# Optimization experiments

Measured on AMD Instinct MI355X. Metric: run time of the kernel, lower is better.

## Reference

```python
import jax, jax.numpy as jnp
import numpy as np

N_NODES = 50000
N_EDGES = 500000
D_MODEL = 256
N_HEADS = 8
D_K = D_MODEL // N_HEADS


def setup_inputs() -> dict:
    key = jax.random.key(0)
    ks = jax.random.split(key, 12)
    s = 1.0 / np.sqrt(D_MODEL)
    inp = {
        "query": jax.random.normal(ks[0], (N_NODES, D_MODEL), dtype=jnp.float32),
        "key": jax.random.normal(ks[1], (N_NODES, D_MODEL), dtype=jnp.float32),
        "value": jax.random.normal(ks[2], (N_NODES, D_MODEL), dtype=jnp.float32),
        "edges": jax.random.randint(ks[3], (2, N_EDGES), 0, N_NODES, dtype=jnp.int64),
        # four nn.Linear(d_model, d_model) layers: q, k, v, out
        "Wq": jax.random.uniform(ks[4], (D_MODEL, D_MODEL), jnp.float32, -s, s),
        "bq": jax.random.uniform(ks[5], (D_MODEL,), jnp.float32, -s, s),
        "Wk": jax.random.uniform(ks[6], (D_MODEL, D_MODEL), jnp.float32, -s, s),
        "bk": jax.random.uniform(ks[7], (D_MODEL,), jnp.float32, -s, s),
        "Wv": jax.random.uniform(ks[8], (D_MODEL, D_MODEL), jnp.float32, -s, s),
        "bv": jax.random.uniform(ks[9], (D_MODEL,), jnp.float32, -s, s),
        "Wo": jax.random.uniform(ks[10], (D_MODEL, D_MODEL), jnp.float32, -s, s),
        "bo": jax.random.uniform(ks[11], (D_MODEL,), jnp.float32, -s, s),
    }
    return inp


def reference(query, key, value, edges, Wq, bq, Wk, bk, Wv, bv, Wo, bo):
    N = query.shape[0]
    # linear projections (torch Linear: x @ W.T + b), view as [N, h, d_k]
    q = (query @ Wq.T + bq).reshape(N, N_HEADS, D_K)
    k = (key @ Wk.T + bk).reshape(N, N_HEADS, D_K)
    v = (value @ Wv.T + bv).reshape(N, N_HEADS, D_K)

    dst, src = edges[0], edges[1]
    # per-edge dot-product scores [E, h]
    scores = jnp.einsum("ehd,ehd->eh", q[dst], k[src]) / jnp.sqrt(
        jnp.asarray(D_K, dtype=q.dtype)
    )
    # segment softmax over destination node neighborhoods (per head)
    m = jax.ops.segment_max(scores, dst, num_segments=N)  # [N, h]
    ex = jnp.exp(scores - m[dst])
    den = jax.ops.segment_sum(ex, dst, num_segments=N)  # [N, h]
    p_attn = ex / den[dst]  # [E, h]

    # weighted scatter-sum of gathered values -> [N, h, d_k]
    out = jax.ops.segment_sum(p_attn[:, :, None] * v[src], dst, num_segments=N)
    out = out.reshape(N, D_MODEL)
    return out @ Wo.T + bo
```

## Files before the change

### kernel.cpp

```cpp
#include <hip/hip_runtime.h>
#include <hip/hip_bf16.h>
#include <cstdint>

#define D_MODEL 256
#define NHEADS 8
#define DK 32
#define LDSPAD 8
#define LDSROW (D_MODEL + LDSPAD)
#define LDSROWF (D_MODEL + 4)
#define PBLK 170

typedef float f32x4 __attribute__((ext_vector_type(4)));
typedef __bf16 bf16x8 __attribute__((ext_vector_type(8)));
typedef unsigned short u16x8 __attribute__((ext_vector_type(8)));

__device__ __forceinline__ unsigned short f2bf_rne(float f) {
    unsigned int u = __float_as_uint(f);
    u += 0x7FFF + ((u >> 16) & 1);
    return (unsigned short)(u >> 16);
}
__device__ __forceinline__ float bf2f(unsigned short h) {
    return __uint_as_float(((unsigned int)h) << 16);
}

__global__ void conv_weights_hist(const float* __restrict__ W0, const float* __restrict__ W1,
                                  const float* __restrict__ W2, const float* __restrict__ W3,
                                  unsigned short* __restrict__ out,
                                  const int* __restrict__ dst, int E,
                                  int* __restrict__ counts) {
    int i = blockIdx.x * blockDim.x + threadIdx.x;
    if (i < 4 * 8192) {
        const int w    = i >> 13;
        const int rem  = i & 8191;
        const int lane = rem & 63;
        const int kk   = (rem >> 6) & 7;
        const int ntile= rem >> 9;
        const int row  = ntile * 16 + (lane & 15);
        const int col  = kk * 32 + (lane >> 4) * 8;
        const float* Wsrc = (w == 0) ? W0 : (w == 1) ? W1 : (w == 2) ? W2 : W3;
        const float* sp = Wsrc + (size_t)row * D_MODEL + col;
        float4 x0 = *(const float4*)sp;
        float4 x1 = *(const float4*)(sp + 4);
        unsigned short* dp = out + (size_t)w * D_MODEL * D_MODEL + (size_t)rem * 8;
        ushort4 o0, o1;
        o0.x = f2bf_rne(x0.x); o0.y = f2bf_rne(x0.y); o0.z = f2bf_rne(x0.z); o0.w = f2bf_rne(x0.w);
        o1.x = f2bf_rne(x1.x); o1.y = f2bf_rne(x1.y); o1.z = f2bf_rne(x1.z); o1.w = f2bf_rne(x1.w);
        *(ushort4*)dp = o0;
        *(ushort4*)(dp + 4) = o1;
    } else {
        const int e = i - 4 * 8192;
        if (e < E) atomicAdd(&counts[dst[e]], 1);
    }
}

__global__ __launch_bounds__(256, 2) void gemm_qkv(
    const float* __restrict__ Aq, const float* __restrict__ Ak, const float* __restrict__ Av,
    const unsigned short* __restrict__ Wsw,
    const float* __restrict__ bq, const float* __restrict__ bk, const float* __restrict__ bv,
    unsigned short* __restrict__ qbuf, unsigned short* __restrict__ kvbuf,
    int M, int mtiles)
{
    __shared__ __align__(16) unsigned short smem[32 * LDSROW];

    const int which = blockIdx.y;
    const float* A = (which == 0) ? Aq : (which == 1) ? Ak : Av;
    const float* bias = (which == 0) ? bq : (which == 1) ? bk : bv;
    const unsigned short* Wb = Wsw + (size_t)which * D_MODEL * D_MODEL;
    unsigned short* outp = (which == 0) ? qbuf : kvbuf;
    const int voff = (which == 2) ? 4 : 0;

    const int lane  = threadIdx.x & 63;
    const int wave  = threadIdx.x >> 6;
    const int mrow  = lane & 15;
    const int quad  = lane >> 4;

    bf16x8 bfr[4][8];
#pragma unroll
    for (int ni = 0; ni < 4; ++ni)
#pragma unroll
        for (int kk = 0; kk < 8; ++kk)
            bfr[ni][kk] = *(const bf16x8*)(Wb + ((size_t)((wave * 4 + ni) * 8 + kk) * 64 + lane) * 8);

    float bcol[4];
#pragma unroll
    for (int ni = 0; ni < 4; ++ni) bcol[ni] = bias[wave * 64 + ni * 16 + mrow];

    for (int t = blockIdx.x; t < mtiles; t += PBLK) {
        const int m0 = t * 32;

#pragma unroll
        for (int i = 0; i < 8; ++i) {
            const int g = i * 256 + threadIdx.x;
            const int r = g >> 6, c4 = g & 63;
            const int grow = min(m0 + r, M - 1);
            float4 x = *(const float4*)(A + (size_t)grow * D_MODEL + c4 * 4);
            ushort4 o;
            o.x = f2bf_rne(x.x); o.y = f2bf_rne(x.y);
            o.z = f2bf_rne(x.z); o.w = f2bf_rne(x.w);
            *(ushort4*)(smem + r * LDSROW + c4 * 4) = o;
        }
        __syncthreads();

        f32x4 acc[2][4] = {};
#pragma unroll
        for (int kk = 0; kk < 8; ++kk) {
            bf16x8 afr[2];
#pragma unroll
            for (int mi = 0; mi < 2; ++mi)
                afr[mi] = *(const bf16x8*)(smem + (mi * 16 + mrow) * LDSROW + kk * 32 + quad * 8);
#pragma unroll
            for (int mi = 0; mi < 2; ++mi)
#pragma unroll
                for (int ni = 0; ni < 4; ++ni)
                    acc[mi][ni] = __builtin_amdgcn_mfma_f32_16x16x32_bf16(
                        afr[mi], bfr[ni][kk], acc[mi][ni], 0, 0, 0);
        }

        __syncthreads();
#pragma unroll
        for (int ni = 0; ni < 4; ++ni) {
            const int col = wave * 64 + ni * 16 + mrow;
#pragma unroll
            for (int mi = 0; mi < 2; ++mi)
#pragma unroll
                for (int r = 0; r < 4; ++r)
                    smem[(mi * 16 + quad * 4 + r) * LDSROW + col] =
                        f2bf_rne(acc[mi][ni][r] + bcol[ni]);
        }
        __syncthreads();
#pragma unroll
        for (int i = 0; i < 4; ++i) {
            const int g = i * 256 + threadIdx.x;
            const int r = g >> 5, c8 = g & 31;
            const int grow = m0 + r;
            if (grow < M) {
                if (which == 0) {
                    bf16x8 x = *(const bf16x8*)(smem + r * LDSROW + c8 * 8);
                    *(bf16x8*)(outp + (size_t)grow * D_MODEL + c8 * 8) = x;
                } else {
                    ushort4 lo = *(const ushort4*)(smem + r * LDSROW + c8 * 8);
                    ushort4 hi = *(const ushort4*)(smem + r * LDSROW + c8 * 8 + 4);
                    unsigned short* base = outp + (size_t)grow * 512 + 16 * c8 + voff;
                    *(ushort4*)base = lo;
                    *(ushort4*)(base + 8) = hi;
                }
            }
        }
        __syncthreads();
    }
}

__global__ __launch_bounds__(256, 2) void gemm_out(
    const unsigned short* __restrict__ Ab, const unsigned short* __restrict__ Wb,
    const float* __restrict__ bias, float* __restrict__ outp, int M, int mtiles)
{
    __shared__ __align__(16) char smem_raw[32 * LDSROWF * 4];
    unsigned short* smemA = (unsigned short*)smem_raw;
    float*          smemF = (float*)smem_raw;

    const int lane  = threadIdx.x & 63;
    const int wave  = threadIdx.x >> 6;
    const int mrow  = lane & 15;
    const int quad  = lane >> 4;

    bf16x8 bfr[4][8];
#pragma unroll
    for (int ni = 0; ni < 4; ++ni)
#pragma unroll
        for (int kk = 0; kk < 8; ++kk)
            bfr[ni][kk] = *(const bf16x8*)(Wb + ((size_t)((wave * 4 + ni) * 8 + kk) * 64 + lane) * 8);

    float bcol[4];
#pragma unroll
    for (int ni = 0; ni < 4; ++ni) bcol[ni] = bias[wave * 64 + ni * 16 + mrow];

    for (int t = blockIdx.x; t < mtiles; t += 3 * PBLK) {
        const int m0 = t * 32;

#pragma unroll
        for (int i = 0; i < 4; ++i) {
            const int g = i * 256 + threadIdx.x;
            const int r = g >> 5, c8 = g & 31;
            const int grow = min(m0 + r, M - 1);
            bf16x8 x = *(const bf16x8*)(Ab + (size_t)grow * D_MODEL + c8 * 8);
            *(bf16x8*)(smemA + r * LDSROW + c8 * 8) = x;
        }
        __syncthreads();

        f32x4 acc[2][4] = {};
#pragma unroll
        for (int kk = 0; kk < 8; ++kk) {
            bf16x8 afr[2];
#pragma unroll
            for (int mi = 0; mi < 2; ++mi)
                afr[mi] = *(const bf16x8*)(smemA + (mi * 16 + mrow) * LDSROW + kk * 32 + quad * 8);
#pragma unroll
            for (int mi = 0; mi < 2; ++mi)
#pragma unroll
                for (int ni = 0; ni < 4; ++ni)
                    acc[mi][ni] = __builtin_amdgcn_mfma_f32_16x16x32_bf16(
                        afr[mi], bfr[ni][kk], acc[mi][ni], 0, 0, 0);
        }

        __syncthreads();
#pragma unroll
        for (int ni = 0; ni < 4; ++ni) {
            const int col = wave * 64 + ni * 16 + mrow;
#pragma unroll
            for (int mi = 0; mi < 2; ++mi)
#pragma unroll
                for (int r = 0; r < 4; ++r)
                    smemF[(mi * 16 + quad * 4 + r) * LDSROWF + col] = acc[mi][ni][r] + bcol[ni];
        }
        __syncthreads();
#pragma unroll
        for (int i = 0; i < 8; ++i) {
            const int g = i * 256 + threadIdx.x;
            const int r = g >> 6, c4 = g & 63;
            const int grow = m0 + r;
            if (grow < M) {
                float4 x = *(const float4*)(smemF + r * LDSROWF + c4 * 4);
                *(float4*)(outp + (size_t)grow * D_MODEL + c4 * 4) = x;
            }
        }
        __syncthreads();
    }
}

__global__ void block_reduce_kernel(const int* __restrict__ counts, int N,
                                    int* __restrict__ blockSums) {
    const int g = blockIdx.x * 256 + threadIdx.x;
    int v = (g < N) ? counts[g] : 0;
#pragma unroll
    for (int d = 1; d < 64; d <<= 1) v += __shfl_xor(v, d);
    __shared__ int ws[4];
    if ((threadIdx.x & 63) == 0) ws[threadIdx.x >> 6] = v;
    __syncthreads();
    if (threadIdx.x == 0) blockSums[blockIdx.x] = ws[0] + ws[1] + ws[2] + ws[3];
}

__global__ void scan_blocks_kernel(int* __restrict__ blockSums, int G) {
    __shared__ int sh[256];
    const int t = threadIdx.x;
    int v = (t < G) ? blockSums[t] : 0;
    sh[t] = v;
    __syncthreads();
#pragma unroll
    for (int off = 1; off < 256; off <<= 1) {
        int add = (t >= off) ? sh[t - off] : 0;
        __syncthreads();
        sh[t] += add;
        __syncthreads();
    }
    if (t < G) blockSums[t] = sh[t] - v;
}

__global__ void scan_write_kernel(const int* __restrict__ counts, int N,
                                  const int* __restrict__ blockOffsets,
                                  int* __restrict__ offsets) {
    const int g = blockIdx.x * 256 + threadIdx.x;
    const int t = threadIdx.x;
    int v = (g < N) ? counts[g] : 0;
    __shared__ int sh[256];
    sh[t] = v;
    __syncthreads();
#pragma unroll
    for (int off = 1; off < 256; off <<= 1) {
        int add = (t >= off) ? sh[t - off] : 0;
        __syncthreads();
        sh[t] += add;
        __syncthreads();
    }
    if (g <= N) offsets[g] = sh[t] - v + blockOffsets[blockIdx.x];
}

__global__ void fill_kernel(const int* __restrict__ dst, const int* __restrict__ src, int E,
                            const int* __restrict__ offsets, int* __restrict__ cursor,
                            int* __restrict__ ssrc) {
    int i = blockIdx.x * blockDim.x + threadIdx.x;
    if (i < E) {
        int d = dst[i];
        int r = atomicAdd(&cursor[d], 1);
        ssrc[offsets[d] + r] = src[i];
    }
}

__global__ __launch_bounds__(256) void attn_kernel(
    const unsigned short* __restrict__ qb, const unsigned short* __restrict__ kv,
    const int* __restrict__ offsets, const int* __restrict__ ssrc,
    unsigned short* __restrict__ attn, int N)
{
    const int node = blockIdx.x * 4 + (threadIdx.x >> 6);
    if (node >= N) return;
    const int lane = threadIdx.x & 63;

    ushort4 qu = *(const ushort4*)(qb + (size_t)node * D_MODEL + 4 * lane);
    const float sc = 0.17677669529663689f;
    float qx = bf2f(qu.x) * sc, qy = bf2f(qu.y) * sc,
          qz = bf2f(qu.z) * sc, qw = bf2f(qu.w) * sc;

    float m = -INFINITY, l = 0.f;
    float ax = 0.f, ay = 0.f, az = 0.f, aw = 0.f;

    const int e0 = offsets[node], e1 = offsets[node + 1];
    int e = e0;

    for (; e + 7 < e1; e += 8) {
        u16x8 a0 = *(const u16x8*)(kv + (size_t)ssrc[e]     * 512 + 8 * lane);
        u16x8 a1 = *(const u16x8*)(kv + (size_t)ssrc[e + 1] * 512 + 8 * lane);
        u16x8 a2 = *(const u16x8*)(kv + (size_t)ssrc[e + 2] * 512 + 8 * lane);
        u16x8 a3 = *(const u16x8*)(kv + (size_t)ssrc[e + 3] * 512 + 8 * lane);
        u16x8 a4 = *(const u16x8*)(kv + (size_t)ssrc[e + 4] * 512 + 8 * lane);
        u16x8 a5 = *(const u16x8*)(kv + (size_t)ssrc[e + 5] * 512 + 8 * lane);
        u16x8 a6 = *(const u16x8*)(kv + (size_t)ssrc[e + 6] * 512 + 8 * lane);
        u16x8 a7 = *(const u16x8*)(kv + (size_t)ssrc[e + 7] * 512 + 8 * lane);

        float p0 = qx * bf2f(a0[0]) + qy * bf2f(a0[1]) + qz * bf2f(a0[2]) + qw * bf2f(a0[3]);
        float p1 = qx * bf2f(a1[0]) + qy * bf2f(a1[1]) + qz * bf2f(a1[2]) + qw * bf2f(a1[3]);
        float p2 = qx * bf2f(a2[0]) + qy * bf2f(a2[1]) + qz * bf2f(a2[2]) + qw * bf2f(a2[3]);
        float p3 = qx * bf2f(a3[0]) + qy * bf2f(a3[1]) + qz * bf2f(a3[2]) + qw * bf2f(a3[3]);
        float p4 = qx * bf2f(a4[0]) + qy * bf2f(a4[1]) + qz * bf2f(a4[2]) + qw * bf2f(a4[3]);
        float p5 = qx * bf2f(a5[0]) + qy * bf2f(a5[1]) + qz * bf2f(a5[2]) + qw * bf2f(a5[3]);
        float p6 = qx * bf2f(a6[0]) + qy * bf2f(a6[1]) + qz * bf2f(a6[2]) + qw * bf2f(a6[3]);
        float p7 = qx * bf2f(a7[0]) + qy * bf2f(a7[1]) + qz * bf2f(a7[2]) + qw * bf2f(a7[3]);
#pragma unroll
        for (int d = 1; d <= 4; d <<= 1) {
            p0 += __shfl_xor(p0, d); p1 += __shfl_xor(p1, d);
            p2 += __shfl_xor(p2, d); p3 += __shfl_xor(p3, d);
            p4 += __shfl_xor(p4, d); p5 += __shfl_xor(p5, d);
            p6 += __shfl_xor(p6, d); p7 += __shfl_xor(p7, d);
        }
        float mnew = fmaxf(fmaxf(fmaxf(fmaxf(m, p0), fmaxf(p1, p2)), fmaxf(fmaxf(p3, p4), fmaxf(p5, p6))), p7);
        float alpha = __expf(m - mnew);
        float w0 = __expf(p0 - mnew), w1 = __expf(p1 - mnew);
        float w2 = __expf(p2 - mnew), w3 = __expf(p3 - mnew);
        float w4 = __expf(p4 - mnew), w5 = __expf(p5 - mnew);
        float w6 = __expf(p6 - mnew), w7 = __expf(p7 - mnew);
        ax = ax * alpha + w0 * bf2f(a0[4]) + w1 * bf2f(a1[4]) + w2 * bf2f(a2[4]) + w3 * bf2f(a3[4])
                        + w4 * bf2f(a4[4]) + w5 * bf2f(a5[4]) + w6 * bf2f(a6[4]) + w7 * bf2f(a7[4]);
        ay = ay * alpha + w0 * bf2f(a0[5]) + w1 * bf2f(a1[5]) + w2 * bf2f(a2[5]) + w3 * bf2f(a3[5])
                        + w4 * bf2f(a4[5]) + w5 * bf2f(a5[5]) + w6 * bf2f(a6[5]) + w7 * bf2f(a7[5]);
        az = az * alpha + w0 * bf2f(a0[6]) + w1 * bf2f(a1[6]) + w2 * bf2f(a2[6]) + w3 * bf2f(a3[6])
                        + w4 * bf2f(a4[6]) + w5 * bf2f(a5[6]) + w6 * bf2f(a6[6]) + w7 * bf2f(a7[6]);
        aw = aw * alpha + w0 * bf2f(a0[7]) + w1 * bf2f(a1[7]) + w2 * bf2f(a2[7]) + w3 * bf2f(a3[7])
                        + w4 * bf2f(a4[7]) + w5 * bf2f(a5[7]) + w6 * bf2f(a6[7]) + w7 * bf2f(a7[7]);
        l = l * alpha + w0 + w1 + w2 + w3 + w4 + w5 + w6 + w7;
        m = mnew;
    }

    for (; e + 3 < e1; e += 4) {
        u16x8 a0 = *(const u16x8*)(kv + (size_t)ssrc[e]     * 512 + 8 * lane);
        u16x8 a1 = *(const u16x8*)(kv + (size_t)ssrc[e + 1] * 512 + 8 * lane);
        u16x8 a2 = *(const u16x8*)(kv + (size_t)ssrc[e + 2] * 512 + 8 * lane);
        u16x8 a3 = *(const u16x8*)(kv + (size_t)ssrc[e + 3] * 512 + 8 * lane);

        float p0 = qx * bf2f(a0[0]) + qy * bf2f(a0[1]) + qz * bf2f(a0[2]) + qw * bf2f(a0[3]);
        float p1 = qx * bf2f(a1[0]) + qy * bf2f(a1[1]) + qz * bf2f(a1[2]) + qw * bf2f(a1[3]);
        float p2 = qx * bf2f(a2[0]) + qy * bf2f(a2[1]) + qz * bf2f(a2[2]) + qw * bf2f(a2[3]);
        float p3 = qx * bf2f(a3[0]) + qy * bf2f(a3[1]) + qz * bf2f(a3[2]) + qw * bf2f(a3[3]);
#pragma unroll
        for (int d = 1; d <= 4; d <<= 1) {
            p0 += __shfl_xor(p0, d); p1 += __shfl_xor(p1, d);
            p2 += __shfl_xor(p2, d); p3 += __shfl_xor(p3, d);
        }
        float mnew = fmaxf(fmaxf(fmaxf(m, p0), fmaxf(p1, p2)), p3);
        float alpha = __expf(m - mnew);
        float w0 = __expf(p0 - mnew), w1 = __expf(p1 - mnew);
        float w2 = __expf(p2 - mnew), w3 = __expf(p3 - mnew);
        ax = ax * alpha + w0 * bf2f(a0[4]) + w1 * bf2f(a1[4]) + w2 * bf2f(a2[4]) + w3 * bf2f(a3[4]);
        ay = ay * alpha + w0 * bf2f(a0[5]) + w1 * bf2f(a1[5]) + w2 * bf2f(a2[5]) + w3 * bf2f(a3[5]);
        az = az * alpha + w0 * bf2f(a0[6]) + w1 * bf2f(a1[6]) + w2 * bf2f(a2[6]) + w3 * bf2f(a3[6]);
        aw = aw * alpha + w0 * bf2f(a0[7]) + w1 * bf2f(a1[7]) + w2 * bf2f(a2[7]) + w3 * bf2f(a3[7]);
        l = l * alpha + w0 + w1 + w2 + w3;
        m = mnew;
    }

    for (; e < e1; ++e) {
        int s = ssrc[e];
        u16x8 a = *(const u16x8*)(kv + (size_t)s * 512 + 8 * lane);
        float p = qx * bf2f(a[0]) + qy * bf2f(a[1]) + qz * bf2f(a[2]) + qw * bf2f(a[3]);
        p += __shfl_xor(p, 1);
        p += __shfl_xor(p, 2);
        p += __shfl_xor(p, 4);
        float mnew  = fmaxf(m, p);
        float alpha = __expf(m - mnew);
        float w     = __expf(p - mnew);
        ax = ax * alpha + w * bf2f(a[4]);
        ay = ay * alpha + w * bf2f(a[5]);
        az = az * alpha + w * bf2f(a[6]);
        aw = aw * alpha + w * bf2f(a[7]);
        l = l * alpha + w;
        m = mnew;
    }

    const float inv = (l > 0.f) ? 1.f / l : 0.f;
    ushort4 o;
    o.x = f2bf_rne(ax * inv);
    o.y = f2bf_rne(ay * inv);
    o.z = f2bf_rne(az * inv);
    o.w = f2bf_rne(aw * inv);
    *(ushort4*)(attn + (size_t)node * D_MODEL + 4 * lane) = o;
}

extern "C" void kernel_launch(void* const* d_in, const int* in_sizes, int n_in,
                              void* d_out, int out_size, void* d_ws, size_t ws_size,
                              hipStream_t stream)
{
    const float* query = (const float*)d_in[0];
    const float* key   = (const float*)d_in[1];
    const float* value = (const float*)d_in[2];
    const int*   edges = (const int*)d_in[3];
    const float* Wq = (const float*)d_in[4];
    const float* bq = (const float*)d_in[5];
    const float* Wk = (const float*)d_in[6];
    const float* bk = (const float*)d_in[7];
    const float* Wv = (const float*)d_in[8];
    const float* bv = (const float*)d_in[9];
    const float* Wo = (const float*)d_in[10];
    const float* bo = (const float*)d_in[11];
    float* out = (float*)d_out;

    const int N = in_sizes[0] / D_MODEL;
    const int E = in_sizes[3] / 2;
    const int* dst = edges;
    const int* src = edges + E;

    char* ws = (char*)d_ws;
    size_t off = 0;
    auto alloc = [&](size_t bytes) {
        void* p = ws + off;
        off += (bytes + 255) & ~(size_t)255;
        return p;
    };
    unsigned short* qbuf  = (unsigned short*)alloc((size_t)N * D_MODEL * 2);
    unsigned short* kvbuf = (unsigned short*)alloc((size_t)N * 2 * D_MODEL * 2);
    unsigned short* attnb = (unsigned short*)alloc((size_t)N * D_MODEL * 2);
    unsigned short* Wbuf  = (unsigned short*)alloc((size_t)4 * D_MODEL * D_MODEL * 2);
    int*            counts  = (int*)alloc((size_t)2 * N * 4);
    int*            offsets = (int*)alloc((size_t)(N + 1) * 4);
    int*            ssrc    = (int*)alloc((size_t)E * 4);
    int*            bsums   = (int*)alloc((size_t)256 * 4);

    hipMemsetAsync(counts, 0, (size_t)2 * N * 4, stream);

    const int fused_threads = 4 * 8192 + E;
    conv_weights_hist<<<(fused_threads + 255) / 256, 256, 0, stream>>>(
        Wq, Wk, Wv, Wo, Wbuf, dst, E, counts);

    const int mtiles = (N + 31) / 32;
    gemm_qkv<<<dim3(PBLK, 3), 256, 0, stream>>>(query, key, value, Wbuf,
                                                bq, bk, bv, qbuf, kvbuf, N, mtiles);

    const int G = (N + 256) / 256;
    block_reduce_kernel<<<G, 256, 0, stream>>>(counts, N, bsums);
    scan_blocks_kernel<<<1, 256, 0, stream>>>(bsums, G);
    scan_write_kernel<<<G, 256, 0, stream>>>(counts, N, bsums, offsets);

    const int eblocks = (E + 255) / 256;
    fill_kernel<<<eblocks, 256, 0, stream>>>(dst, src, E, offsets, counts + N, ssrc);
    attn_kernel<<<(N + 3) / 4, 256, 0, stream>>>(qbuf, kvbuf, offsets, ssrc, attnb, N);

    gemm_out<<<3 * PBLK, 256, 0, stream>>>(attnb, Wbuf + 3 * D_MODEL * D_MODEL, bo, out, N, mtiles);
}
```

Measured before the change: 369.6 us.

## Restructure projection GEMMs to one 64-row tile per block and split KV layout

Both projection GEMMs drop the persistent grid-stride loop for a one-shot grid of 64-row tiles with 512 threads (8 waves, each owning 32 output columns). Results are written straight from accumulators to global memory instead of being staged through LDS, which removes several barriers but makes the stores scattered 2-byte or 4-byte writes. The K/V buffer changes from per-lane interleaving to K and V stored as separate 256-wide halves of each row, so the attention kernel now issues two 8-byte gathers per edge instead of one 16-byte gather. LDS padding is also reduced.

```diff
diff --git a/kernel.cpp b/kernel.cpp
--- a/kernel.cpp
+++ b/kernel.cpp
@@ -5,14 +5,12 @@
 #define D_MODEL 256
 #define NHEADS 8
 #define DK 32
-#define LDSPAD 8
+#define LDSPAD 4
 #define LDSROW (D_MODEL + LDSPAD)
-#define LDSROWF (D_MODEL + 4)
-#define PBLK 170
+#define BM 64
 
 typedef float f32x4 __attribute__((ext_vector_type(4)));
 typedef __bf16 bf16x8 __attribute__((ext_vector_type(8)));
-typedef unsigned short u16x8 __attribute__((ext_vector_type(8)));
 
 __device__ __forceinline__ unsigned short f2bf_rne(float f) {
     unsigned int u = __float_as_uint(f);
@@ -53,178 +51,151 @@
     }
 }
 
-__global__ __launch_bounds__(256, 2) void gemm_qkv(
+__global__ __launch_bounds__(512, 4) void gemm_qkv(
     const float* __restrict__ Aq, const float* __restrict__ Ak, const float* __restrict__ Av,
     const unsigned short* __restrict__ Wsw,
     const float* __restrict__ bq, const float* __restrict__ bk, const float* __restrict__ bv,
     unsigned short* __restrict__ qbuf, unsigned short* __restrict__ kvbuf,
-    int M, int mtiles)
+    int M)
 {
-    __shared__ __align__(16) unsigned short smem[32 * LDSROW];
+    __shared__ __align__(16) unsigned short smem[BM * LDSROW];
 
     const int which = blockIdx.y;
     const float* A = (which == 0) ? Aq : (which == 1) ? Ak : Av;
     const float* bias = (which == 0) ? bq : (which == 1) ? bk : bv;
     const unsigned short* Wb = Wsw + (size_t)which * D_MODEL * D_MODEL;
     unsigned short* outp = (which == 0) ? qbuf : kvbuf;
-    const int voff = (which == 2) ? 4 : 0;
+    const int out_stride = (which == 0) ? D_MODEL : 2 * D_MODEL;
+    const int out_off    = (which == 2) ? D_MODEL : 0;
 
     const int lane  = threadIdx.x & 63;
     const int wave  = threadIdx.x >> 6;
     const int mrow  = lane & 15;
     const int quad  = lane >> 4;
-
-    bf16x8 bfr[4][8];
-#pragma unroll
-    for (int ni = 0; ni < 4; ++ni)
+    const int m0    = blockIdx.x * BM;
+
+    bf16x8 bfr[2][8];
+#pragma unroll
+    for (int ni = 0; ni < 2; ++ni)
 #pragma unroll
         for (int kk = 0; kk < 8; ++kk)
-            bfr[ni][kk] = *(const bf16x8*)(Wb + ((size_t)((wave * 4 + ni) * 8 + kk) * 64 + lane) * 8);
-
-    float bcol[4];
-#pragma unroll
-    for (int ni = 0; ni < 4; ++ni) bcol[ni] = bias[wave * 64 + ni * 16 + mrow];
-
-    for (int t = blockIdx.x; t < mtiles; t += PBLK) {
-        const int m0 = t * 32;
-
-#pragma unroll
-        for (int i = 0; i < 8; ++i) {
-            const int g = i * 256 + threadIdx.x;
+            bfr[ni][kk] = *(const bf16x8*)(Wb + ((size_t)((wave * 2 + ni) * 8 + kk) * 64 + lane) * 8);
+
+    float bcol[2];
+#pragma unroll
+    for (int ni = 0; ni < 2; ++ni) bcol[ni] = bias[wave * 32 + ni * 16 + mrow];
+
+#pragma unroll
+    for (int half = 0; half < 2; ++half) {
+        float4 x[4];
+#pragma unroll
+        for (int i = 0; i < 4; ++i) {
+            const int g = (half * 4 + i) * 512 + threadIdx.x;
             const int r = g >> 6, c4 = g & 63;
             const int grow = min(m0 + r, M - 1);
-            float4 x = *(const float4*)(A + (size_t)grow * D_MODEL + c4 * 4);
+            x[i] = *(const float4*)(A + (size_t)grow * D_MODEL + c4 * 4);
+        }
+#pragma unroll
+        for (int i = 0; i < 4; ++i) {
+            const int g = (half * 4 + i) * 512 + threadIdx.x;
+            const int r = g >> 6, c4 = g & 63;
             ushort4 o;
-            o.x = f2bf_rne(x.x); o.y = f2bf_rne(x.y);
-            o.z = f2bf_rne(x.z); o.w = f2bf_rne(x.w);
+            o.x = f2bf_rne(x[i].x); o.y = f2bf_rne(x[i].y);
+            o.z = f2bf_rne(x[i].z); o.w = f2bf_rne(x[i].w);
             *(ushort4*)(smem + r * LDSROW + c4 * 4) = o;
         }
-        __syncthreads();
-
-        f32x4 acc[2][4] = {};
-#pragma unroll
-        for (int kk = 0; kk < 8; ++kk) {
-            bf16x8 afr[2];
-#pragma unroll
-            for (int mi = 0; mi < 2; ++mi)
-                afr[mi] = *(const bf16x8*)(smem + (mi * 16 + mrow) * LDSROW + kk * 32 + quad * 8);
-#pragma unroll
-            for (int mi = 0; mi < 2; ++mi)
-#pragma unroll
-                for (int ni = 0; ni < 4; ++ni)
-                    acc[mi][ni] = __builtin_amdgcn_mfma_f32_16x16x32_bf16(
-                        afr[mi], bfr[ni][kk], acc[mi][ni], 0, 0, 0);
-        }
-
-        __syncthreads();
-#pragma unroll
-        for (int ni = 0; ni < 4; ++ni) {
-            const int col = wave * 64 + ni * 16 + mrow;
-#pragma unroll
-            for (int mi = 0; mi < 2; ++mi)
-#pragma unroll
-                for (int r = 0; r < 4; ++r)
-                    smem[(mi * 16 + quad * 4 + r) * LDSROW + col] =
+    }
+    __syncthreads();
+
+    f32x4 acc[4][2] = {};
+#pragma unroll
+    for (int kk = 0; kk < 8; ++kk) {
+        bf16x8 afr[4];
+#pragma unroll
+        for (int mi = 0; mi < 4; ++mi)
+            afr[mi] = *(const bf16x8*)(smem + (mi * 16 + mrow) * LDSROW + kk * 32 + quad * 8);
+#pragma unroll
+        for (int mi = 0; mi < 4; ++mi)
+#pragma unroll
+            for (int ni = 0; ni < 2; ++ni)
+                acc[mi][ni] = __builtin_amdgcn_mfma_f32_16x16x32_bf16(
+                    afr[mi], bfr[ni][kk], acc[mi][ni], 0, 0, 0);
+    }
+
+#pragma unroll
+    for (int mi = 0; mi < 4; ++mi)
+#pragma unroll
+        for (int r = 0; r < 4; ++r) {
+            const int row = m0 + mi * 16 + quad * 4 + r;
+            if (row < M) {
+#pragma unroll
+                for (int ni = 0; ni < 2; ++ni)
+                    outp[(size_t)row * out_stride + out_off + wave * 32 + ni * 16 + mrow] =
                         f2bf_rne(acc[mi][ni][r] + bcol[ni]);
-        }
-        __syncthreads();
-#pragma unroll
-        for (int i = 0; i < 4; ++i) {
-            const int g = i * 256 + threadIdx.x;
-            const int r = g >> 5, c8 = g & 31;
-            const int grow = m0 + r;
-            if (grow < M) {
-                if (which == 0) {
-                    bf16x8 x = *(const bf16x8*)(smem + r * LDSROW + c8 * 8);
-                    *(bf16x8*)(outp + (size_t)grow * D_MODEL + c8 * 8) = x;
-                } else {
-                    ushort4 lo = *(const ushort4*)(smem + r * LDSROW + c8 * 8);
-                    ushort4 hi = *(const ushort4*)(smem + r * LDSROW + c8 * 8 + 4);
-                    unsigned short* base = outp + (size_t)grow * 512 + 16 * c8 + voff;
-                    *(ushort4*)base = lo;
-                    *(ushort4*)(base + 8) = hi;
-                }
             }
         }
-        __syncthreads();
-    }
-}
-
-__global__ __launch_bounds__(256, 2) void gemm_out(
+}
+
+__global__ __launch_bounds__(512, 4) void gemm_out(
     const unsigned short* __restrict__ Ab, const unsigned short* __restrict__ Wb,
-    const float* __restrict__ bias, float* __restrict__ outp, int M, int mtiles)
+    const float* __restrict__ bias, float* __restrict__ outp, int M)
 {
-    __shared__ __align__(16) char smem_raw[32 * LDSROWF * 4];
-    unsigned short* smemA = (unsigned short*)smem_raw;
-    float*          smemF = (float*)smem_raw;
+    __shared__ __align__(16) unsigned short smem[BM * LDSROW];
 
     const int lane  = threadIdx.x & 63;
     const int wave  = threadIdx.x >> 6;
     const int mrow  = lane & 15;
     const int quad  = lane >> 4;
-
-    bf16x8 bfr[4][8];
-#pragma unroll
-    for (int ni = 0; ni < 4; ++ni)
+    const int m0    = blockIdx.x * BM;
+
+    bf16x8 bfr[2][8];
+#pragma unroll
+    for (int ni = 0; ni < 2; ++ni)
 #pragma unroll
         for (int kk = 0; kk < 8; ++kk)
-            bfr[ni][kk] = *(const bf16x8*)(Wb + ((size_t)((wave * 4 + ni) * 8 + kk) * 64 + lane) * 8);
-
-    float bcol[4];
-#pragma unroll
-    for (int ni = 0; ni < 4; ++ni) bcol[ni] = bias[wave * 64 + ni * 16 + mrow];
-
-    for (int t = blockIdx.x; t < mtiles; t += 3 * PBLK) {
-        const int m0 = t * 32;
-
-#pragma unroll
-        for (int i = 0; i < 4; ++i) {
-            const int g = i * 256 + threadIdx.x;
-            const int r = g >> 5, c8 = g & 31;
-            const int grow = min(m0 + r, M - 1);
-            bf16x8 x = *(const bf16x8*)(Ab + (size_t)grow * D_MODEL + c8 * 8);
-            *(bf16x8*)(smemA + r * LDSROW + c8 * 8) = x;
-        }
-        __syncthreads();
-
-        f32x4 acc[2][4] = {};
-#pragma unroll
-        for (int kk = 0; kk < 8; ++kk) {
-            bf16x8 afr[2];
-#pragma unroll
-            for (int mi = 0; mi < 2; ++mi)
-                afr[mi] = *(const bf16x8*)(smemA + (mi * 16 + mrow) * LDSROW + kk * 32 + quad * 8);
-#pragma unroll
-            for (int mi = 0; mi < 2; ++mi)
-#pragma unroll
-                for (int ni = 0; ni < 4; ++ni)
-                    acc[mi][ni] = __builtin_amdgcn_mfma_f32_16x16x32_bf16(
-                        afr[mi], bfr[ni][kk], acc[mi][ni], 0, 0, 0);
-        }
-
-        __syncthreads();
-#pragma unroll
-        for (int ni = 0; ni < 4; ++ni) {
-            const int col = wave * 64 + ni * 16 + mrow;
-#pragma unroll
-            for (int mi = 0; mi < 2; ++mi)
-#pragma unroll
-                for (int r = 0; r < 4; ++r)
-                    smemF[(mi * 16 + quad * 4 + r) * LDSROWF + col] = acc[mi][ni][r] + bcol[ni];
-        }
-        __syncthreads();
-#pragma unroll
-        for (int i = 0; i < 8; ++i) {
-            const int g = i * 256 + threadIdx.x;
-            const int r = g >> 6, c4 = g & 63;
-            const int grow = m0 + r;
-            if (grow < M) {
-                float4 x = *(const float4*)(smemF + r * LDSROWF + c4 * 4);
-                *(float4*)(outp + (size_t)grow * D_MODEL + c4 * 4) = x;
+            bfr[ni][kk] = *(const bf16x8*)(Wb + ((size_t)((wave * 2 + ni) * 8 + kk) * 64 + lane) * 8);
+
+    float bcol[2];
+#pragma unroll
+    for (int ni = 0; ni < 2; ++ni) bcol[ni] = bias[wave * 32 + ni * 16 + mrow];
+
+#pragma unroll
+    for (int i = 0; i < 4; ++i) {
+        const int g = i * 512 + threadIdx.x;
+        const int r = g >> 5, c8 = g & 31;
+        const int grow = min(m0 + r, M - 1);
+        bf16x8 x = *(const bf16x8*)(Ab + (size_t)grow * D_MODEL + c8 * 8);
+        *(bf16x8*)(smem + r * LDSROW + c8 * 8) = x;
+    }
+    __syncthreads();
+
+    f32x4 acc[4][2] = {};
+#pragma unroll
+    for (int kk = 0; kk < 8; ++kk) {
+        bf16x8 afr[4];
+#pragma unroll
+        for (int mi = 0; mi < 4; ++mi)
+            afr[mi] = *(const bf16x8*)(smem + (mi * 16 + mrow) * LDSROW + kk * 32 + quad * 8);
+#pragma unroll
+        for (int mi = 0; mi < 4; ++mi)
+#pragma unroll
+            for (int ni = 0; ni < 2; ++ni)
+                acc[mi][ni] = __builtin_amdgcn_mfma_f32_16x16x32_bf16(
+                    afr[mi], bfr[ni][kk], acc[mi][ni], 0, 0, 0);
+    }
+
+#pragma unroll
+    for (int mi = 0; mi < 4; ++mi)
+#pragma unroll
+        for (int r = 0; r < 4; ++r) {
+            const int row = m0 + mi * 16 + quad * 4 + r;
+            if (row < M) {
+#pragma unroll
+                for (int ni = 0; ni < 2; ++ni)
+                    outp[(size_t)row * D_MODEL + wave * 32 + ni * 16 + mrow] =
+                        acc[mi][ni][r] + bcol[ni];
             }
         }
-        __syncthreads();
-    }
 }
 
 __global__ void block_reduce_kernel(const int* __restrict__ counts, int N,
@@ -306,23 +277,31 @@
     int e = e0;
 
     for (; e + 7 < e1; e += 8) {
-        u16x8 a0 = *(const u16x8*)(kv + (size_t)ssrc[e]     * 512 + 8 * lane);
-        u16x8 a1 = *(const u16x8*)(kv + (size_t)ssrc[e + 1] * 512 + 8 * lane);
-        u16x8 a2 = *(const u16x8*)(kv + (size_t)ssrc[e + 2] * 512 + 8 * lane);
-        u16x8 a3 = *(const u16x8*)(kv + (size_t)ssrc[e + 3] * 512 + 8 * lane);
-        u16x8 a4 = *(const u16x8*)(kv + (size_t)ssrc[e + 4] * 512 + 8 * lane);
-        u16x8 a5 = *(const u16x8*)(kv + (size_t)ssrc[e + 5] * 512 + 8 * lane);
-        u16x8 a6 = *(const u16x8*)(kv + (size_t)ssrc[e + 6] * 512 + 8 * lane);
-        u16x8 a7 = *(const u16x8*)(kv + (size_t)ssrc[e + 7] * 512 + 8 * lane);
-
-        float p0 = qx * bf2f(a0[0]) + qy * bf2f(a0[1]) + qz * bf2f(a0[2]) + qw * bf2f(a0[3]);
-        float p1 = qx * bf2f(a1[0]) + qy * bf2f(a1[1]) + qz * bf2f(a1[2]) + qw * bf2f(a1[3]);
-        float p2 = qx * bf2f(a2[0]) + qy * bf2f(a2[1]) + qz * bf2f(a2[2]) + qw * bf2f(a2[3]);
-        float p3 = qx * bf2f(a3[0]) + qy * bf2f(a3[1]) + qz * bf2f(a3[2]) + qw * bf2f(a3[3]);
-        float p4 = qx * bf2f(a4[0]) + qy * bf2f(a4[1]) + qz * bf2f(a4[2]) + qw * bf2f(a4[3]);
-        float p5 = qx * bf2f(a5[0]) + qy * bf2f(a5[1]) + qz * bf2f(a5[2]) + qw * bf2f(a5[3]);
-        float p6 = qx * bf2f(a6[0]) + qy * bf2f(a6[1]) + qz * bf2f(a6[2]) + qw * bf2f(a6[3]);
-        float p7 = qx * bf2f(a7[0]) + qy * bf2f(a7[1]) + qz * bf2f(a7[2]) + qw * bf2f(a7[3]);
+        const unsigned short* b0 = kv + (size_t)ssrc[e]     * 512 + 4 * lane;
+        const unsigned short* b1 = kv + (size_t)ssrc[e + 1] * 512 + 4 * lane;
+        const unsigned short* b2 = kv + (size_t)ssrc[e + 2] * 512 + 4 * lane;
+        const unsigned short* b3 = kv + (size_t)ssrc[e + 3] * 512 + 4 * lane;
+        const unsigned short* b4 = kv + (size_t)ssrc[e + 4] * 512 + 4 * lane;
+        const unsigned short* b5 = kv + (size_t)ssrc[e + 5] * 512 + 4 * lane;
+        const unsigned short* b6 = kv + (size_t)ssrc[e + 6] * 512 + 4 * lane;
+        const unsigned short* b7 = kv + (size_t)ssrc[e + 7] * 512 + 4 * lane;
+        ushort4 k0 = *(const ushort4*)b0, v0 = *(const ushort4*)(b0 + D_MODEL);
+        ushort4 k1 = *(const ushort4*)b1, v1 = *(const ushort4*)(b1 + D_MODEL);
+        ushort4 k2 = *(const ushort4*)b2, v2 = *(const ushort4*)(b2 + D_MODEL);
+        ushort4 k3 = *(const ushort4*)b3, v3 = *(const ushort4*)(b3 + D_MODEL);
+        ushort4 k4 = *(const ushort4*)b4, v4 = *(const ushort4*)(b4 + D_MODEL);
+        ushort4 k5 = *(const ushort4*)b5, v5 = *(const ushort4*)(b5 + D_MODEL);
+        ushort4 k6 = *(const ushort4*)b6, v6 = *(const ushort4*)(b6 + D_MODEL);
+        ushort4 k7 = *(const ushort4*)b7, v7 = *(const ushort4*)(b7 + D_MODEL);
+
+        float p0 = qx * bf2f(k0.x) + qy * bf2f(k0.y) + qz * bf2f(k0.z) + qw * bf2f(k0.w);
+        float p1 = qx * bf2f(k1.x) + qy * bf2f(k1.y) + qz * bf2f(k1.z) + qw * bf2f(k1.w);
+        float p2 = qx * bf2f(k2.x) + qy * bf2f(k2.y) + qz * bf2f(k2.z) + qw * bf2f(k2.w);
+        float p3 = qx * bf2f(k3.x) + qy * bf2f(k3.y) + qz * bf2f(k3.z) + qw * bf2f(k3.w);
+        float p4 = qx * bf2f(k4.x) + qy * bf2f(k4.y) + qz * bf2f(k4.z) + qw * bf2f(k4.w);
+        float p5 = qx * bf2f(k5.x) + qy * bf2f(k5.y) + qz * bf2f(k5.z) + qw * bf2f(k5.w);
+        float p6 = qx * bf2f(k6.x) + qy * bf2f(k6.y) + qz * bf2f(k6.z) + qw * bf2f(k6.w);
+        float p7 = qx * bf2f(k7.x) + qy * bf2f(k7.y) + qz * bf2f(k7.z) + qw * bf2f(k7.w);
 #pragma unroll
         for (int d = 1; d <= 4; d <<= 1) {
             p0 += __shfl_xor(p0, d); p1 += __shfl_xor(p1, d);
@@ -336,28 +315,32 @@
         float w2 = __expf(p2 - mnew), w3 = __expf(p3 - mnew);
         float w4 = __expf(p4 - mnew), w5 = __expf(p5 - mnew);
         float w6 = __expf(p6 - mnew), w7 = __expf(p7 - mnew);
-        ax = ax * alpha + w0 * bf2f(a0[4]) + w1 * bf2f(a1[4]) + w2 * bf2f(a2[4]) + w3 * bf2f(a3[4])
-                        + w4 * bf2f(a4[4]) + w5 * bf2f(a5[4]) + w6 * bf2f(a6[4]) + w7 * bf2f(a7[4]);
-        ay = ay * alpha + w0 * bf2f(a0[5]) + w1 * bf2f(a1[5]) + w2 * bf2f(a2[5]) + w3 * bf2f(a3[5])
-                        + w4 * bf2f(a4[5]) + w5 * bf2f(a5[5]) + w6 * bf2f(a6[5]) + w7 * bf2f(a7[5]);
-        az = az * alpha + w0 * bf2f(a0[6]) + w1 * bf2f(a1[6]) + w2 * bf2f(a2[6]) + w3 * bf2f(a3[6])
-                        + w4 * bf2f(a4[6]) + w5 * bf2f(a5[6]) + w6 * bf2f(a6[6]) + w7 * bf2f(a7[6]);
-        aw = aw * alpha + w0 * bf2f(a0[7]) + w1 * bf2f(a1[7]) + w2 * bf2f(a2[7]) + w3 * bf2f(a3[7])
-                        + w4 * bf2f(a4[7]) + w5 * bf2f(a5[7]) + w6 * bf2f(a6[7]) + w7 * bf2f(a7[7]);
+        ax = ax * alpha + w0 * bf2f(v0.x) + w1 * bf2f(v1.x) + w2 * bf2f(v2.x) + w3 * bf2f(v3.x)
+                        + w4 * bf2f(v4.x) + w5 * bf2f(v5.x) + w6 * bf2f(v6.x) + w7 * bf2f(v7.x);
+        ay = ay * alpha + w0 * bf2f(v0.y) + w1 * bf2f(v1.y) + w2 * bf2f(v2.y) + w3 * bf2f(v3.y)
+                        + w4 * bf2f(v4.y) + w5 * bf2f(v5.y) + w6 * bf2f(v6.y) + w7 * bf2f(v7.y);
+        az = az * alpha + w0 * bf2f(v0.z) + w1 * bf2f(v1.z) + w2 * bf2f(v2.z) + w3 * bf2f(v3.z)
+                        + w4 * bf2f(v4.z) + w5 * bf2f(v5.z) + w6 * bf2f(v6.z) + w7 * bf2f(v7.z);
+        aw = aw * alpha + w0 * bf2f(v0.w) + w1 * bf2f(v1.w) + w2 * bf2f(v2.w) + w3 * bf2f(v3.w)
+                        + w4 * bf2f(v4.w) + w5 * bf2f(v5.w) + w6 * bf2f(v6.w) + w7 * bf2f(v7.w);
         l = l * alpha + w0 + w1 + w2 + w3 + w4 + w5 + w6 + w7;
         m = mnew;
     }
 
     for (; e + 3 < e1; e += 4) {
-        u16x8 a0 = *(const u16x8*)(kv + (size_t)ssrc[e]     * 512 + 8 * lane);
-        u16x8 a1 = *(const u16x8*)(kv + (size_t)ssrc[e + 1] * 512 + 8 * lane);
-        u16x8 a2 = *(const u16x8*)(kv + (size_t)ssrc[e + 2] * 512 + 8 * lane);
-        u16x8 a3 = *(const u16x8*)(kv + (size_t)ssrc[e + 3] * 512 + 8 * lane);
-
-        float p0 = qx * bf2f(a0[0]) + qy * bf2f(a0[1]) + qz * bf2f(a0[2]) + qw * bf2f(a0[3]);
-        float p1 = qx * bf2f(a1[0]) + qy * bf2f(a1[1]) + qz * bf2f(a1[2]) + qw * bf2f(a1[3]);
-        float p2 = qx * bf2f(a2[0]) + qy * bf2f(a2[1]) + qz * bf2f(a2[2]) + qw * bf2f(a2[3]);
-        float p3 = qx * bf2f(a3[0]) + qy * bf2f(a3[1]) + qz * bf2f(a3[2]) + qw * bf2f(a3[3]);
+        const unsigned short* b0 = kv + (size_t)ssrc[e]     * 512 + 4 * lane;
+        const unsigned short* b1 = kv + (size_t)ssrc[e + 1] * 512 + 4 * lane;
+        const unsigned short* b2 = kv + (size_t)ssrc[e + 2] * 512 + 4 * lane;
+        const unsigned short* b3 = kv + (size_t)ssrc[e + 3] * 512 + 4 * lane;
+        ushort4 k0 = *(const ushort4*)b0, v0 = *(const ushort4*)(b0 + D_MODEL);
+        ushort4 k1 = *(const ushort4*)b1, v1 = *(const ushort4*)(b1 + D_MODEL);
+        ushort4 k2 = *(const ushort4*)b2, v2 = *(const ushort4*)(b2 + D_MODEL);
+        ushort4 k3 = *(const ushort4*)b3, v3 = *(const ushort4*)(b3 + D_MODEL);
+
+        float p0 = qx * bf2f(k0.x) + qy * bf2f(k0.y) + qz * bf2f(k0.z) + qw * bf2f(k0.w);
+        float p1 = qx * bf2f(k1.x) + qy * bf2f(k1.y) + qz * bf2f(k1.z) + qw * bf2f(k1.w);
+        float p2 = qx * bf2f(k2.x) + qy * bf2f(k2.y) + qz * bf2f(k2.z) + qw * bf2f(k2.w);
+        float p3 = qx * bf2f(k3.x) + qy * bf2f(k3.y) + qz * bf2f(k3.z) + qw * bf2f(k3.w);
 #pragma unroll
         for (int d = 1; d <= 4; d <<= 1) {
             p0 += __shfl_xor(p0, d); p1 += __shfl_xor(p1, d);
@@ -367,28 +350,29 @@
         float alpha = __expf(m - mnew);
         float w0 = __expf(p0 - mnew), w1 = __expf(p1 - mnew);
         float w2 = __expf(p2 - mnew), w3 = __expf(p3 - mnew);
-        ax = ax * alpha + w0 * bf2f(a0[4]) + w1 * bf2f(a1[4]) + w2 * bf2f(a2[4]) + w3 * bf2f(a3[4]);
-        ay = ay * alpha + w0 * bf2f(a0[5]) + w1 * bf2f(a1[5]) + w2 * bf2f(a2[5]) + w3 * bf2f(a3[5]);
-        az = az * alpha + w0 * bf2f(a0[6]) + w1 * bf2f(a1[6]) + w2 * bf2f(a2[6]) + w3 * bf2f(a3[6]);
-        aw = aw * alpha + w0 * bf2f(a0[7]) + w1 * bf2f(a1[7]) + w2 * bf2f(a2[7]) + w3 * bf2f(a3[7]);
+        ax = ax * alpha + w0 * bf2f(v0.x) + w1 * bf2f(v1.x) + w2 * bf2f(v2.x) + w3 * bf2f(v3.x);
+        ay = ay * alpha + w0 * bf2f(v0.y) + w1 * bf2f(v1.y) + w2 * bf2f(v2.y) + w3 * bf2f(v3.y);
+        az = az * alpha + w0 * bf2f(v0.z) + w1 * bf2f(v1.z) + w2 * bf2f(v2.z) + w3 * bf2f(v3.z);
+        aw = aw * alpha + w0 * bf2f(v0.w) + w1 * bf2f(v1.w) + w2 * bf2f(v2.w) + w3 * bf2f(v3.w);
         l = l * alpha + w0 + w1 + w2 + w3;
         m = mnew;
     }
 
     for (; e < e1; ++e) {
-        int s = ssrc[e];
-        u16x8 a = *(const u16x8*)(kv + (size_t)s * 512 + 8 * lane);
-        float p = qx * bf2f(a[0]) + qy * bf2f(a[1]) + qz * bf2f(a[2]) + qw * bf2f(a[3]);
+        const unsigned short* b = kv + (size_t)ssrc[e] * 512 + 4 * lane;
+        ushort4 ku = *(const ushort4*)b;
+        ushort4 vu = *(const ushort4*)(b + D_MODEL);
+        float p = qx * bf2f(ku.x) + qy * bf2f(ku.y) + qz * bf2f(ku.z) + qw * bf2f(ku.w);
         p += __shfl_xor(p, 1);
         p += __shfl_xor(p, 2);
         p += __shfl_xor(p, 4);
         float mnew  = fmaxf(m, p);
         float alpha = __expf(m - mnew);
         float w     = __expf(p - mnew);
-        ax = ax * alpha + w * bf2f(a[4]);
-        ay = ay * alpha + w * bf2f(a[5]);
-        az = az * alpha + w * bf2f(a[6]);
-        aw = aw * alpha + w * bf2f(a[7]);
+        ax = ax * alpha + w * bf2f(vu.x);
+        ay = ay * alpha + w * bf2f(vu.y);
+        az = az * alpha + w * bf2f(vu.z);
+        aw = aw * alpha + w * bf2f(vu.w);
         l = l * alpha + w;
         m = mnew;
     }
@@ -447,9 +431,9 @@
     conv_weights_hist<<<(fused_threads + 255) / 256, 256, 0, stream>>>(
         Wq, Wk, Wv, Wo, Wbuf, dst, E, counts);
 
-    const int mtiles = (N + 31) / 32;
-    gemm_qkv<<<dim3(PBLK, 3), 256, 0, stream>>>(query, key, value, Wbuf,
-                                                bq, bk, bv, qbuf, kvbuf, N, mtiles);
+    const int mtiles = (N + BM - 1) / BM;
+    gemm_qkv<<<dim3(mtiles, 3), 512, 0, stream>>>(query, key, value, Wbuf,
+                                                  bq, bk, bv, qbuf, kvbuf, N);
 
     const int G = (N + 256) / 256;
     block_reduce_kernel<<<G, 256, 0, stream>>>(counts, N, bsums);
@@ -460,5 +444,5 @@
     fill_kernel<<<eblocks, 256, 0, stream>>>(dst, src, E, offsets, counts + N, ssrc);
     attn_kernel<<<(N + 3) / 4, 256, 0, stream>>>(qbuf, kvbuf, offsets, ssrc, attnb, N);
 
-    gemm_out<<<3 * PBLK, 256, 0, stream>>>(attnb, Wbuf + 3 * D_MODEL * D_MODEL, bo, out, N, mtiles);
-}
+    gemm_out<<<mtiles, 512, 0, stream>>>(attnb, Wbuf + 3 * D_MODEL * D_MODEL, bo, out, N);
+}
```

Measured after the change: 371.5 us. No clear change (+0.5%).
